# Performance work log

Hardware: AMD Instinct MI355X
Metric: run time of the kernel (lower is better)

## Reference

```python
import jax, jax.numpy as jnp
import numpy as np

NUM_HEADS = 16
EMBED_DIM = 1024
BSZ, T, S = 8, 1024, 1024
NEG_INF = -1e30


def setup_inputs() -> dict:
    key = jax.random.key(0)
    ks = jax.random.split(key, 12)
    E = EMBED_DIM
    decoder_state = jax.random.normal(ks[0], (BSZ, T, E), dtype=jnp.float32)
    source_hids = jax.random.normal(ks[1], (S, BSZ, E), dtype=jnp.float32)
    # realistic padding mask: True = padded position (masked out)
    lengths = jax.random.randint(ks[2], (BSZ,), S // 2, S + 1)
    src_len_mask = jnp.arange(S)[None, :] >= lengths[:, None]  # (BSZ, S) bool
    init = 1.0 / np.sqrt(E)
    Wq = jax.random.uniform(ks[3], (E, E), minval=-init, maxval=init)
    bq = jax.random.uniform(ks[4], (E,), minval=-init, maxval=init)
    Wk = jax.random.uniform(ks[5], (E, E), minval=-init, maxval=init)
    bk = jax.random.uniform(ks[6], (E,), minval=-init, maxval=init)
    Wv = jax.random.uniform(ks[7], (E, E), minval=-init, maxval=init)
    bv = jax.random.uniform(ks[8], (E,), minval=-init, maxval=init)
    Wo = jax.random.uniform(ks[9], (E, E), minval=-init, maxval=init)
    bo = jax.random.uniform(ks[10], (E,), minval=-init, maxval=init)
    return {"decoder_state": decoder_state, "source_hids": source_hids,
            "src_len_mask": src_len_mask, "Wq": Wq, "bq": bq, "Wk": Wk,
            "bk": bk, "Wv": Wv, "bv": bv, "Wo": Wo, "bo": bo}


def reference(decoder_state, source_hids, src_len_mask, Wq, bq, Wk, bk, Wv, bv, Wo, bo):
    B, Tq, E = decoder_state.shape
    Sk = source_hids.shape[0]
    H = NUM_HEADS
    hd = E // H
    scaling = hd ** (-0.5)

    query = jnp.swapaxes(decoder_state, 0, 1)  # (T, B, E)
    q = (query @ Wq.T + bq) * scaling          # (T, B, E)
    k = source_hids @ Wk.T + bk                # (S, B, E)
    v = source_hids @ Wv.T + bv                # (S, B, E)

    q = q.reshape(Tq, B, H, hd)
    k = k.reshape(Sk, B, H, hd)
    v = v.reshape(Sk, B, H, hd)

    scores = jnp.einsum("tbhd,sbhd->bhts", q, k)  # (B, H, T, S)
    scores = jnp.where(src_len_mask[:, None, None, :], NEG_INF, scores)
    weights = jax.nn.softmax(scores, axis=-1)     # (B, H, T, S); dropout p=0

    attn = jnp.einsum("bhts,sbhd->tbhd", weights, v).reshape(Tq, B, E)
    attn = attn @ Wo.T + bo                       # (T, B, E)

    # need_weights: mean over heads -> (B, T, S); then transpose(0,2) -> (S, T, B)
    attn_weights_out = jnp.swapaxes(weights.mean(axis=1), 0, 2)
    # squeeze=True is a no-op here since T != 1
    return attn, attn_weights_out
```

## Files before the change

### kernel.cpp

```cpp
#include <hip/hip_runtime.h>
#include <stdint.h>
#include <stddef.h>

typedef __attribute__((ext_vector_type(8))) short bf16x8;
typedef __attribute__((ext_vector_type(4))) float f32x4;
typedef __attribute__((ext_vector_type(4))) uint32_t u32x4;

#define DEVINL static __device__ __forceinline__

DEVINL float b2f(uint16_t u) {
  uint32_t x = ((uint32_t)u) << 16;
  float f;
  __builtin_memcpy(&f, &x, 4);
  return f;
}

DEVINL uint16_t f2b(float f) {
  uint32_t u;
  __builtin_memcpy(&u, &f, 4);
  return (uint16_t)((u + 0x7fffu + ((u >> 16) & 1u)) >> 16);
}

DEVINL void gload16(const void* gsrc, void* ldst) {
  __builtin_amdgcn_global_load_lds(
      (const __attribute__((address_space(1))) void*)gsrc,
      (__attribute__((address_space(3))) void*)ldst, 16, 0, 0);
}

__global__ void detect_kernel(const void* __restrict__ wq, const void* __restrict__ mask,
                              const void* __restrict__ bq, const void* __restrict__ bk,
                              const void* __restrict__ bv, const void* __restrict__ bo,
                              int* __restrict__ hdr, float* __restrict__ bias) {
  __shared__ int sflag, smask32, slen[8];
  const int tid = threadIdx.x;
  if (tid == 0) { sflag = 0; smask32 = 0; }
  if (tid < 8) slen[tid] = 0;
  __syncthreads();
  const uint16_t* w16 = (const uint16_t*)wq;
  int f = 0;
  for (int i = tid; i < 4096; i += 256) {
    uint16_t u = w16[i];
    uint32_t e = (u >> 7) & 0xFFu;
    if (fabsf(b2f(u)) > 0.25f || e == 0xFFu) f = 1;
  }
  if (f) atomicOr(&sflag, 1);
  const uint8_t* mb = (const uint8_t*)mask;
  int m32 = 0;
  for (int i = tid; i < 8191; i += 256) {
    if ((i & 1023) != 1023 && mb[i] != 0 && mb[i + 1] == 0) m32 = 1;
  }
  if (m32) atomicOr(&smask32, 1);
  __syncthreads();
  if (smask32) {
    const int* mi = (const int*)mask;
    for (int i = tid; i < 8192; i += 256) { if (mi[i] == 0) atomicAdd(&slen[i >> 10], 1); }
  } else {
    for (int i = tid; i < 8192; i += 256) { if (mb[i] == 0) atomicAdd(&slen[i >> 10], 1); }
  }
  __syncthreads();
  if (tid == 0) hdr[0] = sflag;
  if (tid < 8) hdr[1 + tid] = slen[tid];
  const void* bs[4] = {bq, bk, bv, bo};
  for (int j = 0; j < 4; ++j) {
    for (int i = tid; i < 1024; i += 256) {
      float v = sflag ? ((const float*)bs[j])[i] : b2f(((const uint16_t*)bs[j])[i]);
      bias[j * 1024 + i] = v;
    }
  }
}

__global__ __launch_bounds__(256)
void convert_kernel(const void* __restrict__ s0, const void* __restrict__ s1,
                    const void* __restrict__ s2, const void* __restrict__ s3,
                    const void* __restrict__ s4, const void* __restrict__ s5,
                    uint16_t* __restrict__ d0, uint16_t* __restrict__ d1,
                    uint16_t* __restrict__ d2, const int* __restrict__ hdr, int doW) {
  const int isf = hdr[0];
  const size_t n01 = 1048576;
  const size_t nw = 131072;
  const size_t total = doW ? (2 * n01 + 4 * nw) : (2 * n01);
  size_t gid = (size_t)blockIdx.x * 256 + threadIdx.x;
  const size_t stride = (size_t)gridDim.x * 256;
  for (; gid < total; gid += stride) {
    const void* sp;
    uint16_t* dp;
    size_t off;
    if (gid < n01) { sp = s0; dp = d0; off = gid; }
    else if (gid < 2 * n01) { sp = s1; dp = d1; off = gid - n01; }
    else {
      const size_t w = (gid - 2 * n01) >> 17;
      off = (gid - 2 * n01) & (nw - 1);
      sp = (w == 0) ? s2 : (w == 1) ? s3 : (w == 2) ? s4 : s5;
      dp = d2 + w * 1048576;
    }
    if (isf) {
      const float* fp = (const float*)sp + off * 8;
      const f32x4 a = *(const f32x4*)fp;
      const f32x4 c = *(const f32x4*)(fp + 4);
      u32x4 r;
      r[0] = (uint32_t)f2b(a[0]) | ((uint32_t)f2b(a[1]) << 16);
      r[1] = (uint32_t)f2b(a[2]) | ((uint32_t)f2b(a[3]) << 16);
      r[2] = (uint32_t)f2b(c[0]) | ((uint32_t)f2b(c[1]) << 16);
      r[3] = (uint32_t)f2b(c[2]) | ((uint32_t)f2b(c[3]) << 16);
      *(u32x4*)(dp + off * 8) = r;
    } else {
      *(u32x4*)(dp + off * 8) = *(const u32x4*)((const uint16_t*)sp + off * 8);
    }
  }
}

enum { MQ = 0, MK = 1, MV = 2, MO = 3 };

DEVINL u32x4 load8w(const void* __restrict__ src, bool f32, size_t eoff) {
  if (!f32) {
    return *(const u32x4*)((const uint16_t*)src + eoff);
  }
  const float* p = (const float*)src + eoff;
  const f32x4 a = *(const f32x4*)p;
  const f32x4 c = *(const f32x4*)(p + 4);
  u32x4 r;
  r[0] = (uint32_t)f2b(a[0]) | ((uint32_t)f2b(a[1]) << 16);
  r[1] = (uint32_t)f2b(a[2]) | ((uint32_t)f2b(a[3]) << 16);
  r[2] = (uint32_t)f2b(c[0]) | ((uint32_t)f2b(c[1]) << 16);
  r[3] = (uint32_t)f2b(c[2]) | ((uint32_t)f2b(c[3]) << 16);
  return r;
}

__global__ __launch_bounds__(256)
void gemm_qkv(const uint16_t* __restrict__ dec_b, const uint16_t* __restrict__ src_b,
              const void* __restrict__ Wq, const void* __restrict__ Wk,
              const void* __restrict__ Wv, const float* __restrict__ bias,
              const int* __restrict__ hdr, uint16_t* __restrict__ Q,
              uint16_t* __restrict__ K, uint16_t* __restrict__ V, int wIsBf16) {
  __shared__ __align__(16) uint16_t lA[8192];
  __shared__ __align__(16) uint16_t lB[8192];
  const int tid = threadIdx.x, lane = tid & 63, wave = tid >> 6;
  const int bm = blockIdx.x;
  const int grp = blockIdx.y >> 3, bn = blockIdx.y & 7;
  const int isf = hdr[0];
  const bool wF32 = (wIsBf16 == 0) && (isf != 0);
  const uint16_t* Ab = (grp == 0) ? dec_b : src_b;
  const void* Wr = (grp == 0) ? Wq : (grp == 1) ? Wk : Wv;
  const float* bs = bias + grp * 1024;
  const float scale = (grp == 0) ? 0.125f : 1.f;
  const int wm = wave >> 1, wn = wave & 1;
  const int g = lane >> 4, cc = lane & 15;
  const int lr = lane >> 3, lc = lane & 7;
  const int scc = (lc ^ lr) * 8;

  f32x4 acc[4][4];
#pragma unroll
  for (int i = 0; i < 4; ++i)
#pragma unroll
    for (int j = 0; j < 4; ++j) acc[i][j] = (f32x4){0.f, 0.f, 0.f, 0.f};

  for (int kt = 0; kt < 16; ++kt) {
    __syncthreads();
#pragma unroll
    for (int q = 0; q < 4; ++q) {
      const int j = wave * 4 + q;
      gload16(Ab + (size_t)(bm * 128 + j * 8 + lr) * 1024 + kt * 64 + scc, &lA[j * 512]);
    }
    if (!wF32) {
#pragma unroll
      for (int q = 0; q < 4; ++q) {
        const int j = wave * 4 + q;
        gload16((const uint16_t*)Wr + (size_t)(bn * 128 + j * 8 + lr) * 1024 + kt * 64 + scc, &lB[j * 512]);
      }
    } else {
#pragma unroll
      for (int q = 0; q < 4; ++q) {
        const int j = wave * 4 + q;
        const u32x4 rv = load8w(Wr, true, (size_t)(bn * 128 + j * 8 + lr) * 1024 + kt * 64 + lc * 8);
        *(u32x4*)&lB[j * 512 + lr * 64 + ((lc ^ lr) * 8)] = rv;
      }
    }
    __syncthreads();
#pragma unroll
    for (int kk = 0; kk < 2; ++kk) {
      bf16x8 af[4], bfr[4];
#pragma unroll
      for (int mi = 0; mi < 4; ++mi) {
        const int row = wm * 64 + mi * 16 + cc;
        af[mi] = *(const bf16x8*)&lA[row * 64 + (((kk * 4 + g) ^ (cc & 7)) << 3)];
      }
#pragma unroll
      for (int ni = 0; ni < 4; ++ni) {
        const int row = wn * 64 + ni * 16 + cc;
        bfr[ni] = *(const bf16x8*)&lB[row * 64 + (((kk * 4 + g) ^ (cc & 7)) << 3)];
      }
#pragma unroll
      for (int mi = 0; mi < 4; ++mi)
#pragma unroll
        for (int ni = 0; ni < 4; ++ni)
          acc[mi][ni] = __builtin_amdgcn_mfma_f32_16x16x32_bf16(af[mi], bfr[ni], acc[mi][ni], 0, 0, 0);
    }
  }
#pragma unroll
  for (int mi = 0; mi < 4; ++mi) {
#pragma unroll
    for (int ni = 0; ni < 4; ++ni) {
      const int col = bn * 128 + wn * 64 + ni * 16 + cc;
      const float bv = bs[col];
      const int r0 = bm * 128 + wm * 64 + mi * 16 + g * 4;
#pragma unroll
      for (int r = 0; r < 4; ++r) {
        const int row = r0 + r;
        const float v = (acc[mi][ni][r] + bv) * scale;
        if (grp == 0) {
          const int b = row >> 10, t = row & 1023, h = col >> 6, d = col & 63;
          Q[(((size_t)(b * 16 + h) << 10) + t) * 64 + d] = f2b(v);
        } else if (grp == 1) {
          const int s = row >> 3, b = row & 7, h = col >> 6, d = col & 63;
          K[(((size_t)(b * 16 + h) << 10) + s) * 64 + d] = f2b(v);
        } else {
          const int s = row >> 3, b = row & 7, h = col >> 6, d = col & 63;
          V[(((size_t)(b * 16 + h) << 6) + d) * 1024 + s] = f2b(v);
        }
      }
    }
  }
}

template <int MODE>
__global__ __launch_bounds__(256)
void gemm_bt(const uint16_t* __restrict__ Ab, const void* __restrict__ Wr,
             const float* __restrict__ bias, const int* __restrict__ hdr,
             void* __restrict__ outp, float scale, int wIsBf16) {
  __shared__ __align__(16) uint16_t lA[8192];
  __shared__ __align__(16) uint16_t lB[8192];
  const int tid = threadIdx.x, lane = tid & 63, wave = tid >> 6;
  const int bm = blockIdx.x, bn = blockIdx.y;
  const int isf = hdr[0];
  const bool wF32 = (wIsBf16 == 0) && (isf != 0);
  const int wm = wave >> 1, wn = wave & 1;
  const int g = lane >> 4, cc = lane & 15;
  const int lr = lane >> 3, lc = lane & 7;
  const int scc = (lc ^ lr) * 8;

  f32x4 acc[4][4];
#pragma unroll
  for (int i = 0; i < 4; ++i)
#pragma unroll
    for (int j = 0; j < 4; ++j) acc[i][j] = (f32x4){0.f, 0.f, 0.f, 0.f};

  for (int kt = 0; kt < 16; ++kt) {
    __syncthreads();
#pragma unroll
    for (int q = 0; q < 4; ++q) {
      const int j = wave * 4 + q;
      gload16(Ab + (size_t)(bm * 128 + j * 8 + lr) * 1024 + kt * 64 + scc, &lA[j * 512]);
    }
    if (!wF32) {
#pragma unroll
      for (int q = 0; q < 4; ++q) {
        const int j = wave * 4 + q;
        gload16((const uint16_t*)Wr + (size_t)(bn * 128 + j * 8 + lr) * 1024 + kt * 64 + scc, &lB[j * 512]);
      }
    } else {
#pragma unroll
      for (int q = 0; q < 4; ++q) {
        const int j = wave * 4 + q;
        const u32x4 rv = load8w(Wr, true, (size_t)(bn * 128 + j * 8 + lr) * 1024 + kt * 64 + lc * 8);
        *(u32x4*)&lB[j * 512 + lr * 64 + ((lc ^ lr) * 8)] = rv;
      }
    }
    __syncthreads();
#pragma unroll
    for (int kk = 0; kk < 2; ++kk) {
      bf16x8 af[4], bfr[4];
#pragma unroll
      for (int mi = 0; mi < 4; ++mi) {
        const int row = wm * 64 + mi * 16 + cc;
        af[mi] = *(const bf16x8*)&lA[row * 64 + (((kk * 4 + g) ^ (cc & 7)) << 3)];
      }
#pragma unroll
      for (int ni = 0; ni < 4; ++ni) {
        const int row = wn * 64 + ni * 16 + cc;
        bfr[ni] = *(const bf16x8*)&lB[row * 64 + (((kk * 4 + g) ^ (cc & 7)) << 3)];
      }
#pragma unroll
      for (int mi = 0; mi < 4; ++mi)
#pragma unroll
        for (int ni = 0; ni < 4; ++ni)
          acc[mi][ni] = __builtin_amdgcn_mfma_f32_16x16x32_bf16(af[mi], bfr[ni], acc[mi][ni], 0, 0, 0);
    }
  }
#pragma unroll
  for (int mi = 0; mi < 4; ++mi) {
#pragma unroll
    for (int ni = 0; ni < 4; ++ni) {
      const int col = bn * 128 + wn * 64 + ni * 16 + cc;
      const float bv = bias[col];
      const int r0 = bm * 128 + wm * 64 + mi * 16 + g * 4;
#pragma unroll
      for (int r = 0; r < 4; ++r) {
        const int row = r0 + r;
        const float v = (acc[mi][ni][r] + bv) * scale;
        const size_t o = (size_t)row * 1024 + col;
        if (isf) ((float*)outp)[o] = v;
        else ((uint16_t*)outp)[o] = f2b(v);
      }
    }
  }
}

__global__ __launch_bounds__(1024)
void attn_kernel(const uint16_t* __restrict__ Qh, const uint16_t* __restrict__ Kh,
                 const uint16_t* __restrict__ Vh, const int* __restrict__ hdr,
                 uint16_t* __restrict__ AP, uint16_t* __restrict__ Wm) {
  __shared__ __align__(16) uint16_t kbuf[2][8192];
  __shared__ __align__(16) uint16_t vbuf[2][8192];
  __shared__ __align__(16) uint16_t pstash[32][1024];
  __shared__ float pvx[2][32][68];

  const int tid = threadIdx.x, lane = tid & 63, w = tid >> 6;
  const int g = lane >> 4, cc = lane & 15;
  const int wt = w >> 3, ws = w & 7;
  const int dq = (w >> 1) & 3, ks = w & 1;
  const int b = blockIdx.x & 7, tt = blockIdx.x >> 3;
  const int t0 = tt * 32;
  const int len = hdr[1 + b];
  const int tme = tid >> 5, s5 = tid & 31;

  auto stage = [&](int p, int buf) {
    const int hh = p >> 3, st = p & 7;
    const uint16_t* Kb = Kh + ((size_t)(b * 16 + hh) << 16);
    const uint16_t* Vt = Vh + ((size_t)(b * 16 + hh) << 16);
    {
      const int row = tid >> 3;
      const int c = (tid & 7) ^ (row & 7);
      gload16(Kb + (st * 128 + row) * 64 + c * 8, &kbuf[buf][w * 512]);
    }
    {
      const int d = tid >> 4;
      const int c = tid & 15;
      const int cg = (c & 8) | ((c ^ (d & 7)) & 7);
      gload16(Vt + d * 1024 + st * 128 + cg * 8, &vbuf[buf][w * 512]);
    }
  };

  stage(0, 0);

  float wmean[32];
#pragma unroll
  for (int j = 0; j < 32; ++j) wmean[j] = 0.f;

  for (int h = 0; h < 16; ++h) {
    const uint16_t* Qb = Qh + ((size_t)(b * 16 + h) << 16) + (((size_t)(t0 + wt * 16 + cc)) << 6);
    const bf16x8 qf0 = *(const bf16x8*)(Qb + g * 8);
    const bf16x8 qf1 = *(const bf16x8*)(Qb + 32 + g * 8);
    f32x4 pv = (f32x4){0.f, 0.f, 0.f, 0.f};
    for (int st = 0; st < 8; ++st) {
      const int p = h * 8 + st;
      const int cur = p & 1;
      asm volatile("s_waitcnt vmcnt(0)" ::: "memory");
      __builtin_amdgcn_sched_barrier(0);
      __builtin_amdgcn_s_barrier();
      if (p + 1 < 128) stage(p + 1, cur ^ 1);
      {
        const int row = ws * 16 + cc;
        f32x4 a = (f32x4){0.f, 0.f, 0.f, 0.f};
#pragma unroll
        for (int kk = 0; kk < 2; ++kk) {
          const bf16x8 kf = *(const bf16x8*)&kbuf[cur][row * 64 + (((kk * 4 + g) ^ (cc & 7)) << 3)];
          a = __builtin_amdgcn_mfma_f32_16x16x32_bf16(kk ? qf1 : qf0, kf, a, 0, 0, 0);
        }
        const int s = st * 128 + row;
        const bool msk = (s >= len);
        float vv0 = msk ? 0.f : __expf(a[0]);
        float vv1 = msk ? 0.f : __expf(a[1]);
        float vv2 = msk ? 0.f : __expf(a[2]);
        float vv3 = msk ? 0.f : __expf(a[3]);
        uint32_t pk01, pk23;
        asm("v_cvt_pk_bf16_f32 %0, %1, %2" : "=v"(pk01) : "v"(vv0), "v"(vv1));
        asm("v_cvt_pk_bf16_f32 %0, %1, %2" : "=v"(pk23) : "v"(vv2), "v"(vv3));
        const uint16_t pb[4] = {(uint16_t)pk01, (uint16_t)(pk01 >> 16),
                                (uint16_t)pk23, (uint16_t)(pk23 >> 16)};
        const int cbase = st * 16 + ws * 2 + (cc >> 3);
#pragma unroll
        for (int r = 0; r < 4; ++r) {
          const int tl = wt * 16 + g * 4 + r;
          const int cs = (cbase & ~7) | ((cbase ^ tl) & 7);
          pstash[tl][(cs << 3) + (cc & 7)] = pb[r];
        }
      }
      asm volatile("s_waitcnt lgkmcnt(0)" ::: "memory");
      __builtin_amdgcn_sched_barrier(0);
      __builtin_amdgcn_s_barrier();
      {
        const int tr = wt * 16 + cc;
#pragma unroll
        for (int kk = 0; kk < 2; ++kk) {
          const int ca = st * 16 + ks * 8 + kk * 4 + g;
          const int ca2 = (ca & ~7) | ((ca ^ tr) & 7);
          const bf16x8 af = *(const bf16x8*)&pstash[tr][ca2 << 3];
          const int cv = ks * 8 + kk * 4 + g;
          const int cv2 = (cv & 8) | ((cv ^ (cc & 7)) & 7);
          const bf16x8 vf = *(const bf16x8*)&vbuf[cur][(dq * 16 + cc) * 128 + (cv2 << 3)];
          pv = __builtin_amdgcn_mfma_f32_16x16x32_bf16(af, vf, pv, 0, 0, 0);
        }
      }
    }
#pragma unroll
    for (int r = 0; r < 4; ++r)
      pvx[ks][wt * 16 + g * 4 + r][dq * 16 + cc] = pv[r];
    float winv;
    {
      uint32_t p4[16];
#pragma unroll
      for (int q = 0; q < 4; ++q) {
        const int c = s5 + 32 * q;
        const int c2 = (c & ~7) | ((c ^ tme) & 7);
        *(u32x4*)&p4[q * 4] = *(const u32x4*)&pstash[tme][c2 << 3];
      }
      float sm = 0.f;
#pragma unroll
      for (int j = 0; j < 16; ++j) {
        sm += b2f((uint16_t)(p4[j] & 0xffffu));
        sm += b2f((uint16_t)(p4[j] >> 16));
      }
#pragma unroll
      for (int m = 16; m >= 1; m >>= 1) sm += __shfl_xor(sm, m, 64);
      winv = 1.f / sm;
#pragma unroll
      for (int j = 0; j < 16; ++j) {
        wmean[2 * j] += b2f((uint16_t)(p4[j] & 0xffffu)) * winv;
        wmean[2 * j + 1] += b2f((uint16_t)(p4[j] >> 16)) * winv;
      }
    }
    asm volatile("s_waitcnt lgkmcnt(0)" ::: "memory");
    __builtin_amdgcn_sched_barrier(0);
    __builtin_amdgcn_s_barrier();
    {
      const int d0 = s5 * 2;
      const float v0 = (pvx[0][tme][d0] + pvx[1][tme][d0]) * winv;
      const float v1 = (pvx[0][tme][d0 + 1] + pvx[1][tme][d0 + 1]) * winv;
      const uint32_t pk = (uint32_t)f2b(v0) | ((uint32_t)f2b(v1) << 16);
      *(uint32_t*)(AP + ((((size_t)(t0 + tme)) * 8 + b) << 10) + h * 64 + d0) = pk;
    }
  }

  {
    uint16_t* dst = Wm + (((size_t)(b * 1024 + t0 + tme)) << 10);
#pragma unroll
    for (int q = 0; q < 4; ++q) {
      uint16_t ob[8];
#pragma unroll
      for (int e = 0; e < 8; ++e) ob[e] = f2b(wmean[q * 8 + e] * 0.0625f);
      *(u32x4*)(dst + q * 256 + s5 * 8) = *(const u32x4*)ob;
    }
  }
}

__global__ __launch_bounds__(256)
void wtrans_kernel(const uint16_t* __restrict__ Wm, const int* __restrict__ hdr,
                   void* __restrict__ outBase) {
  __shared__ uint16_t lt[8][32][68];
  const int tid = threadIdx.x;
  const int s0 = blockIdx.x * 64, t0 = blockIdx.y * 32;
  const int isf = hdr[0];
  const int rr = tid >> 4;
  const int sc = (tid & 15) * 4;
#pragma unroll
  for (int p = 0; p < 16; ++p) {
    const int row = p * 16 + rr;
    const int b = row >> 5, t = row & 31;
    const uint64_t v = *(const uint64_t*)(Wm + (((size_t)(b * 1024 + t0 + t)) << 10) + s0 + sc);
    *(uint64_t*)&lt[b][t][sc] = v;
  }
  __syncthreads();
#pragma unroll
  for (int p = 0; p < 8; ++p) {
    const int pair = p * 256 + tid;
    const int t = pair & 31, s = pair >> 5;
    const size_t o = 8388608 + ((size_t)(s0 + s) * 1024 + (t0 + t)) * 8;
    if (isf) {
      f32x4 v0, v1;
#pragma unroll
      for (int b = 0; b < 4; ++b) v0[b] = b2f(lt[b][t][s]);
#pragma unroll
      for (int b = 0; b < 4; ++b) v1[b] = b2f(lt[b + 4][t][s]);
      *(f32x4*)((float*)outBase + o) = v0;
      *(f32x4*)((float*)outBase + o + 4) = v1;
    } else {
      u32x4 v;
#pragma unroll
      for (int q = 0; q < 4; ++q)
        v[q] = (uint32_t)lt[2 * q][t][s] | ((uint32_t)lt[2 * q + 1][t][s] << 16);
      *(u32x4*)((uint16_t*)outBase + o) = v;
    }
  }
}

__global__ void fill_pattern(uint32_t* p, size_t n) {
  size_t i = (size_t)blockIdx.x * 256 + threadIdx.x;
  const size_t stride = (size_t)gridDim.x * 256;
  for (; i < n; i += stride) p[i] = 0x3f3f3f3fu;
}

extern "C" void kernel_launch(void* const* d_in, const int* in_sizes, int n_in,
                              void* d_out, int out_size, void* d_ws, size_t ws_size,
                              hipStream_t stream) {
  char* ws = (char*)d_ws;
  int* hdr = (int*)ws;
  float* bias = (float*)(ws + 4096);
  uint16_t* Q = (uint16_t*)(ws + (1u << 20));
  uint16_t* K = Q + 8388608;
  uint16_t* V = K + 8388608;
  uint16_t* AP = V + 8388608;
  uint16_t* Wm = AP + 8388608;
  uint16_t* dec_b = AP;
  uint16_t* src_b = Wm;
  const size_t needBase = (1ull << 20) + 5ull * 16777216ull;
  const size_t needFull = needBase + 8ull * 1048576ull;
  uint16_t* Wb = (uint16_t*)(ws + needBase);
  const int useConvW = (ws_size >= needFull) ? 1 : 0;
  if (ws_size < needBase) {
    fill_pattern<<<1024, 256, 0, stream>>>((uint32_t*)d_out, (size_t)out_size / 2);
    return;
  }

  detect_kernel<<<1, 256, 0, stream>>>(d_in[3], d_in[2], d_in[4], d_in[6], d_in[8], d_in[10], hdr, bias);

  convert_kernel<<<4096, 256, 0, stream>>>(d_in[0], d_in[1], d_in[3], d_in[5], d_in[7], d_in[9],
                                           dec_b, src_b, Wb, hdr, useConvW);

  const void* Wq = useConvW ? (const void*)(Wb + 0 * 1048576) : (const void*)d_in[3];
  const void* Wk = useConvW ? (const void*)(Wb + 1 * 1048576) : (const void*)d_in[5];
  const void* Wv = useConvW ? (const void*)(Wb + 2 * 1048576) : (const void*)d_in[7];
  const void* Wo = useConvW ? (const void*)(Wb + 3 * 1048576) : (const void*)d_in[9];

  gemm_qkv<<<dim3(64, 24), 256, 0, stream>>>(dec_b, src_b, Wq, Wk, Wv, bias, hdr, Q, K, V, useConvW);

  attn_kernel<<<256, 1024, 0, stream>>>(Q, K, V, hdr, AP, Wm);

  wtrans_kernel<<<dim3(16, 32), 256, 0, stream>>>(Wm, hdr, d_out);

  gemm_bt<MO><<<dim3(64, 8), 256, 0, stream>>>(AP, Wo, bias + 3072, hdr, d_out, 1.f, useConvW);
}
```

Before: 300.9 us.

## Double-buffer LDS tiles in projection GEMMs to overlap loads with MFMA

The QKV and output projection GEMM kernels now keep two LDS buffers for the A and B tiles. The next k-tile is issued into the alternate buffer before the MFMA work on the current tile runs, with one explicit waitcnt plus barrier per iteration in place of two syncthreads. This aims to hide global-to-LDS load latency behind compute. LDS use doubles to 64KB per block, which may lower occupancy. When weights are fp32, the register-path conversion loads still stall the wave before compute starts.

Result: no change. 302.1 us (+0.4%).

```diff
diff --git a/kernel.cpp b/kernel.cpp
--- a/kernel.cpp
+++ b/kernel.cpp
@@ -132,8 +132,8 @@
               const void* __restrict__ Wv, const float* __restrict__ bias,
               const int* __restrict__ hdr, uint16_t* __restrict__ Q,
               uint16_t* __restrict__ K, uint16_t* __restrict__ V, int wIsBf16) {
-  __shared__ __align__(16) uint16_t lA[8192];
-  __shared__ __align__(16) uint16_t lB[8192];
+  __shared__ __align__(16) uint16_t lA[2][8192];
+  __shared__ __align__(16) uint16_t lB[2][8192];
   const int tid = threadIdx.x, lane = tid & 63, wave = tid >> 6;
   const int bm = blockIdx.x;
   const int grp = blockIdx.y >> 3, bn = blockIdx.y & 7;
@@ -148,46 +148,53 @@
   const int lr = lane >> 3, lc = lane & 7;
   const int scc = (lc ^ lr) * 8;
 
-  f32x4 acc[4][4];
-#pragma unroll
-  for (int i = 0; i < 4; ++i)
-#pragma unroll
-    for (int j = 0; j < 4; ++j) acc[i][j] = (f32x4){0.f, 0.f, 0.f, 0.f};
-
-  for (int kt = 0; kt < 16; ++kt) {
-    __syncthreads();
+  auto stage = [&](int kt, int buf) {
 #pragma unroll
     for (int q = 0; q < 4; ++q) {
       const int j = wave * 4 + q;
-      gload16(Ab + (size_t)(bm * 128 + j * 8 + lr) * 1024 + kt * 64 + scc, &lA[j * 512]);
+      gload16(Ab + (size_t)(bm * 128 + j * 8 + lr) * 1024 + kt * 64 + scc, &lA[buf][j * 512]);
     }
     if (!wF32) {
 #pragma unroll
       for (int q = 0; q < 4; ++q) {
         const int j = wave * 4 + q;
-        gload16((const uint16_t*)Wr + (size_t)(bn * 128 + j * 8 + lr) * 1024 + kt * 64 + scc, &lB[j * 512]);
+        gload16((const uint16_t*)Wr + (size_t)(bn * 128 + j * 8 + lr) * 1024 + kt * 64 + scc, &lB[buf][j * 512]);
       }
     } else {
 #pragma unroll
       for (int q = 0; q < 4; ++q) {
         const int j = wave * 4 + q;
         const u32x4 rv = load8w(Wr, true, (size_t)(bn * 128 + j * 8 + lr) * 1024 + kt * 64 + lc * 8);
-        *(u32x4*)&lB[j * 512 + lr * 64 + ((lc ^ lr) * 8)] = rv;
-      }
-    }
-    __syncthreads();
+        *(u32x4*)&lB[buf][j * 512 + lr * 64 + ((lc ^ lr) * 8)] = rv;
+      }
+    }
+  };
+
+  f32x4 acc[4][4];
+#pragma unroll
+  for (int i = 0; i < 4; ++i)
+#pragma unroll
+    for (int j = 0; j < 4; ++j) acc[i][j] = (f32x4){0.f, 0.f, 0.f, 0.f};
+
+  stage(0, 0);
+  for (int kt = 0; kt < 16; ++kt) {
+    const int cur = kt & 1;
+    asm volatile("s_waitcnt vmcnt(0) lgkmcnt(0)" ::: "memory");
+    __builtin_amdgcn_sched_barrier(0);
+    __builtin_amdgcn_s_barrier();
+    if (kt + 1 < 16) stage(kt + 1, cur ^ 1);
 #pragma unroll
     for (int kk = 0; kk < 2; ++kk) {
       bf16x8 af[4], bfr[4];
 #pragma unroll
       for (int mi = 0; mi < 4; ++mi) {
         const int row = wm * 64 + mi * 16 + cc;
-        af[mi] = *(const bf16x8*)&lA[row * 64 + (((kk * 4 + g) ^ (cc & 7)) << 3)];
+        af[mi] = *(const bf16x8*)&lA[cur][row * 64 + (((kk * 4 + g) ^ (cc & 7)) << 3)];
       }
 #pragma unroll
       for (int ni = 0; ni < 4; ++ni) {
         const int row = wn * 64 + ni * 16 + cc;
-        bfr[ni] = *(const bf16x8*)&lB[row * 64 + (((kk * 4 + g) ^ (cc & 7)) << 3)];
+        bfr[ni] = *(const bf16x8*)&lB[cur][row * 64 + (((kk * 4 + g) ^ (cc & 7)) << 3)];
       }
 #pragma unroll
       for (int mi = 0; mi < 4; ++mi)
@@ -227,8 +234,8 @@
 void gemm_bt(const uint16_t* __restrict__ Ab, const void* __restrict__ Wr,
              const float* __restrict__ bias, const int* __restrict__ hdr,
              void* __restrict__ outp, float scale, int wIsBf16) {
-  __shared__ __align__(16) uint16_t lA[8192];
-  __shared__ __align__(16) uint16_t lB[8192];
+  __shared__ __align__(16) uint16_t lA[2][8192];
+  __shared__ __align__(16) uint16_t lB[2][8192];
   const int tid = threadIdx.x, lane = tid & 63, wave = tid >> 6;
   const int bm = blockIdx.x, bn = blockIdx.y;
   const int isf = hdr[0];
@@ -238,46 +245,53 @@
   const int lr = lane >> 3, lc = lane & 7;
   const int scc = (lc ^ lr) * 8;
 
-  f32x4 acc[4][4];
-#pragma unroll
-  for (int i = 0; i < 4; ++i)
-#pragma unroll
-    for (int j = 0; j < 4; ++j) acc[i][j] = (f32x4){0.f, 0.f, 0.f, 0.f};
-
-  for (int kt = 0; kt < 16; ++kt) {
-    __syncthreads();
+  auto stage = [&](int kt, int buf) {
 #pragma unroll
     for (int q = 0; q < 4; ++q) {
       const int j = wave * 4 + q;
-      gload16(Ab + (size_t)(bm * 128 + j * 8 + lr) * 1024 + kt * 64 + scc, &lA[j * 512]);
+      gload16(Ab + (size_t)(bm * 128 + j * 8 + lr) * 1024 + kt * 64 + scc, &lA[buf][j * 512]);
     }
     if (!wF32) {
 #pragma unroll
       for (int q = 0; q < 4; ++q) {
         const int j = wave * 4 + q;
-        gload16((const uint16_t*)Wr + (size_t)(bn * 128 + j * 8 + lr) * 1024 + kt * 64 + scc, &lB[j * 512]);
+        gload16((const uint16_t*)Wr + (size_t)(bn * 128 + j * 8 + lr) * 1024 + kt * 64 + scc, &lB[buf][j * 512]);
       }
     } else {
 #pragma unroll
       for (int q = 0; q < 4; ++q) {
         const int j = wave * 4 + q;
         const u32x4 rv = load8w(Wr, true, (size_t)(bn * 128 + j * 8 + lr) * 1024 + kt * 64 + lc * 8);
-        *(u32x4*)&lB[j * 512 + lr * 64 + ((lc ^ lr) * 8)] = rv;
-      }
-    }
-    __syncthreads();
+        *(u32x4*)&lB[buf][j * 512 + lr * 64 + ((lc ^ lr) * 8)] = rv;
+      }
+    }
+  };
+
+  f32x4 acc[4][4];
+#pragma unroll
+  for (int i = 0; i < 4; ++i)
+#pragma unroll
+    for (int j = 0; j < 4; ++j) acc[i][j] = (f32x4){0.f, 0.f, 0.f, 0.f};
+
+  stage(0, 0);
+  for (int kt = 0; kt < 16; ++kt) {
+    const int cur = kt & 1;
+    asm volatile("s_waitcnt vmcnt(0) lgkmcnt(0)" ::: "memory");
+    __builtin_amdgcn_sched_barrier(0);
+    __builtin_amdgcn_s_barrier();
+    if (kt + 1 < 16) stage(kt + 1, cur ^ 1);
 #pragma unroll
     for (int kk = 0; kk < 2; ++kk) {
       bf16x8 af[4], bfr[4];
 #pragma unroll
       for (int mi = 0; mi < 4; ++mi) {
         const int row = wm * 64 + mi * 16 + cc;
-        af[mi] = *(const bf16x8*)&lA[row * 64 + (((kk * 4 + g) ^ (cc & 7)) << 3)];
+        af[mi] = *(const bf16x8*)&lA[cur][row * 64 + (((kk * 4 + g) ^ (cc & 7)) << 3)];
       }
 #pragma unroll
       for (int ni = 0; ni < 4; ++ni) {
         const int row = wn * 64 + ni * 16 + cc;
-        bfr[ni] = *(const bf16x8*)&lB[row * 64 + (((kk * 4 + g) ^ (cc & 7)) << 3)];
+        bfr[ni] = *(const bf16x8*)&lB[cur][row * 64 + (((kk * 4 + g) ^ (cc & 7)) << 3)];
       }
 #pragma unroll
       for (int mi = 0; mi < 4; ++mi)
```
